# Kernel tuning notes

Hardware: AMD Instinct MI355X
Metric: run time of the kernel (lower is better)

The kernel has to match this reference:

```python
import jax, jax.numpy as jnp
import numpy as np

B, S, D_MODEL, H = 4, 1024, 1024, 16
HD = D_MODEL // H  # head_dim = 64


def setup_inputs() -> dict:
    key = jax.random.key(0)
    ks = jax.random.split(key, 12)
    sd = 1.0 / np.sqrt(D_MODEL)
    return {
        "x": jax.random.normal(ks[0], (B, S, D_MODEL), dtype=jnp.float32),
        "Wq": jax.random.normal(ks[1], (D_MODEL, D_MODEL), dtype=jnp.float32) * sd,
        "bq": jnp.zeros((D_MODEL,), dtype=jnp.float32),
        "Wk": jax.random.normal(ks[2], (D_MODEL, D_MODEL), dtype=jnp.float32) * sd,
        "bk": jnp.zeros((D_MODEL,), dtype=jnp.float32),
        "Wv": jax.random.normal(ks[3], (D_MODEL, D_MODEL), dtype=jnp.float32) * sd,
        "bv": jnp.zeros((D_MODEL,), dtype=jnp.float32),
        "W1": jax.random.normal(ks[4], (2 * D_MODEL, D_MODEL), dtype=jnp.float32) * sd,
        "b1": jnp.zeros((2 * D_MODEL,), dtype=jnp.float32),
        "W2": jax.random.normal(ks[5], (D_MODEL, 2 * D_MODEL), dtype=jnp.float32) * (1.0 / np.sqrt(2 * D_MODEL)),
        "b2": jnp.zeros((D_MODEL,), dtype=jnp.float32),
        "mask": jnp.ones((B, S, S), dtype=jnp.int32),
    }


def reference(x, Wq, bq, Wk, bk, Wv, bv, W1, b1, W2, b2, mask):
    # QKV projections (torch Linear: y = x @ W.T + b), split into heads -> [B,H,S,HD]
    def proj(W, b):
        return (x @ W.T + b).reshape(B, S, H, HD).transpose(0, 2, 1, 3)

    q = proj(Wq, bq)
    k = proj(Wk, bk)
    v = proj(Wv, bv)

    scores = jnp.einsum("bhqd,bhkd->bhqk", q, k) / jnp.sqrt(jnp.float32(HD))
    # mask [B,S,S] broadcast over heads (original does unsqueeze(1).repeat)
    scores = jnp.where(mask[:, None, :, :] == 0, jnp.float32(-1e8), scores)
    probs = jax.nn.softmax(scores, axis=-1)
    ctx = jnp.einsum("bhqk,bhkd->bhqd", probs, v)
    ctx = ctx.transpose(0, 2, 1, 3).reshape(B, S, D_MODEL)

    # out-projection MLP: Linear(d, 2d) -> ReLU -> Linear(2d, d)
    h = jax.nn.relu(ctx @ W1.T + b1)
    return h @ W2.T + b2
```

## Files before the change

kernel.cpp:

```cpp
#include <hip/hip_runtime.h>
#include <hip/hip_bf16.h>
#include <stdint.h>


#define B_ 4
#define S_ 1024
#define DM_ 1024
#define H_ 16
#define HD_ 64

typedef __attribute__((ext_vector_type(8))) short short8;
typedef __attribute__((ext_vector_type(4))) float f32x4;
typedef __attribute__((ext_vector_type(4))) unsigned short ushort4v;

#define GLB_AS(p) ((const __attribute__((address_space(1))) void*)(p))
#define LDS_AS(p) ((__attribute__((address_space(3))) void*)(p))

__device__ __forceinline__ void async_load16(const void* g, void* l) {
  __builtin_amdgcn_global_load_lds(GLB_AS(g), LDS_AS(l), 16, 0, 0);
}

__device__ __forceinline__ unsigned short f2bf(float x) {
  union { float f; unsigned int u; } v; v.f = x;
  unsigned int r = v.u + 0x7fffu + ((v.u >> 16) & 1u);
  return (unsigned short)(r >> 16);
}

#define QSCALE 0.18033688011112042f

struct ConvArgs {
  const float* src[6];
  unsigned short* dst[6];
  int n4[6];
};

__global__ void convert_bf16_kernel(ConvArgs a) {
  const int seg = blockIdx.y;
  const int n4 = a.n4[seg];
  const f32x4* __restrict__ src = (const f32x4*)a.src[seg];
  ushort4v* __restrict__ dst = (ushort4v*)a.dst[seg];
  for (int i = blockIdx.x * blockDim.x + threadIdx.x; i < n4;
       i += gridDim.x * blockDim.x) {
    f32x4 v = src[i];
    ushort4v o;
    o[0] = f2bf(v[0]); o[1] = f2bf(v[1]); o[2] = f2bf(v[2]); o[3] = f2bf(v[3]);
    dst[i] = o;
  }
}

__global__ void pack_mask_kernel(const int* __restrict__ mask,
                                 unsigned long long* __restrict__ bits,
                                 unsigned int* __restrict__ rowflag) {
  const int row = blockIdx.x * 4 + (threadIdx.x >> 6);
  const int lane = threadIdx.x & 63;
  const int* mr = mask + (size_t)row * S_;
  unsigned long long allf = ~0ull;
#pragma unroll
  for (int g = 0; g < 16; ++g) {
    int mv = mr[g * 64 + lane];
    unsigned long long bal = __ballot(mv != 0);
    if (lane == g) bits[(size_t)row * 16 + g] = bal;
    allf &= bal;
  }
  if (lane == 0) rowflag[row] = (allf == ~0ull) ? 1u : 0u;
}

__global__ void concat_bias_kernel(const float* __restrict__ bq,
                                   const float* __restrict__ bk,
                                   const float* __restrict__ bv,
                                   float* __restrict__ cb) {
  int i = blockIdx.x * 256 + threadIdx.x;
  const float* src = (i < 1024) ? bq : (i < 2048) ? bk : bv;
  cb[i] = src[i & 1023];
}

enum { EPI_QKV = 0, EPI_RELU_BF16 = 2, EPI_F32 = 3, EPI_PARTIAL = 4 };

template <int EPI>
__global__ __launch_bounds__(256, 3) void gemm_bt(
    const unsigned short* __restrict__ A, const unsigned short* __restrict__ Bt,
    const float* __restrict__ bias, void* __restrict__ Cp, int M, int N, int K,
    int Kld) {
  __shared__ unsigned short sA[128 * 64];
  __shared__ unsigned short sB[128 * 64];

  const int tid = threadIdx.x;
  const int lane = tid & 63;
  const int wave = tid >> 6;
  const int quad = lane >> 4;
  const int l15 = lane & 15;
  const int swzb = l15 & 7;
  const int m0 = blockIdx.y * 128;
  const int n0 = blockIdx.x * 128;
  const int wm = (wave >> 1) * 64;
  const int wn = (wave & 1) * 64;
  const int kz = blockIdx.z * K;

  f32x4 acc[4][4];
#pragma unroll
  for (int i = 0; i < 4; ++i)
#pragma unroll
    for (int j = 0; j < 4; ++j) acc[i][j] = (f32x4){0.f, 0.f, 0.f, 0.f};

  const int srow = tid >> 3;
  const int scol = ((tid & 7) ^ (srow & 7)) * 8;
  const unsigned short* gA = A + (size_t)(m0 + srow) * Kld + kz + scol;
  const unsigned short* gB = Bt + (size_t)(n0 + srow) * Kld + kz + scol;
  unsigned short* lA = sA + tid * 8;
  unsigned short* lB = sB + tid * 8;

  for (int k0 = 0; k0 < K; k0 += 64) {
    __syncthreads();
#pragma unroll
    for (int st = 0; st < 4; ++st) {
      async_load16(gA + (size_t)(st * 32) * Kld + k0, lA + st * 2048);
      async_load16(gB + (size_t)(st * 32) * Kld + k0, lB + st * 2048);
    }
    __syncthreads();

#pragma unroll
    for (int ks = 0; ks < 2; ++ks) {
      short8 af[4], bfr[4];
#pragma unroll
      for (int t = 0; t < 4; ++t) {
        const int cg = ((ks * 4 + quad) ^ swzb) * 8;
        af[t] = *(const short8*)(sA + (wm + t * 16 + l15) * 64 + cg);
        bfr[t] = *(const short8*)(sB + (wn + t * 16 + l15) * 64 + cg);
      }
#pragma unroll
      for (int mt = 0; mt < 4; ++mt)
#pragma unroll
        for (int nt = 0; nt < 4; ++nt)
          acc[mt][nt] = __builtin_amdgcn_mfma_f32_16x16x32_bf16(
              af[mt], bfr[nt], acc[mt][nt], 0, 0, 0);
    }
  }

#pragma unroll
  for (int nt = 0; nt < 4; ++nt) {
    const int col = n0 + wn + nt * 16 + l15;
    const float bv = (EPI == EPI_PARTIAL) ? 0.f : bias[col];
    const float scl = (EPI == EPI_QKV && col < 1024) ? QSCALE : 1.0f;
#pragma unroll
    for (int mt = 0; mt < 4; ++mt) {
#pragma unroll
      for (int r = 0; r < 4; ++r) {
        const int row = m0 + wm + mt * 16 + quad * 4 + r;
        float v = acc[mt][nt][r] + bv;
        if (EPI == EPI_F32) {
          ((float*)Cp)[(size_t)row * N + col] = v;
        } else if (EPI == EPI_PARTIAL) {
          ((float*)Cp)[(size_t)blockIdx.z * M * N + (size_t)row * N + col] = v;
        } else if (EPI == EPI_RELU_BF16) {
          ((unsigned short*)Cp)[(size_t)row * N + col] = f2bf(fmaxf(v, 0.f));
        } else {
          ((unsigned short*)Cp)[(size_t)row * N + col] = f2bf(v * scl);
        }
      }
    }
  }
}

__global__ __launch_bounds__(256) void transpose_v(
    const unsigned short* __restrict__ Cqkv, unsigned short* __restrict__ Vt) {
  __shared__ unsigned short t[128 * 65];
  const int bh = blockIdx.x;
  const int stile = blockIdx.y;
  const int b = bh >> 4, h = bh & 15;
  const int tid = threadIdx.x;
  const unsigned short* src =
      Cqkv + ((size_t)(b * S_) + stile * 128) * 3072 + 2048 + h * 64;
#pragma unroll
  for (int ps = 0; ps < 4; ++ps) {
    const int idx = ps * 256 + tid;
    const int r = idx >> 3, c = idx & 7;
    const short8 v = *(const short8*)(src + (size_t)r * 3072 + c * 8);
#pragma unroll
    for (int i = 0; i < 8; ++i) t[r * 65 + c * 8 + i] = (unsigned short)v[i];
  }
  __syncthreads();
  unsigned short* dst = Vt + (size_t)bh * HD_ * S_ + stile * 128;
#pragma unroll
  for (int ps = 0; ps < 4; ++ps) {
    const int idx = ps * 256 + tid;
    const int d = idx >> 4, sc = idx & 15;
    short8 v;
#pragma unroll
    for (int i = 0; i < 8; ++i) v[i] = (short)t[(sc * 8 + i) * 65 + d];
    *(short8*)(dst + (size_t)d * S_ + sc * 8) = v;
  }
}

__global__ __launch_bounds__(256, 2) void flash_attn(
    const unsigned short* __restrict__ Cqkv, const unsigned short* __restrict__ Vt,
    const unsigned long long* __restrict__ mbits,
    const unsigned int* __restrict__ mrowflag,
    unsigned short* __restrict__ ctx) {
  __shared__ unsigned short sK[128 * 64];
  __shared__ unsigned short sV[64 * 128];
  __shared__ unsigned short spb[4][32 * 136];

  const int tid = threadIdx.x;
  const int wave = tid >> 6;
  const int lane = tid & 63;
  const int quad = lane >> 4;
  const int l15 = lane & 15;
  const int bh = blockIdx.x;
  const int b = bh >> 4;
  const int h = bh & 15;
  const int qbase = blockIdx.y * 128 + wave * 32;

  const unsigned short* Qb = Cqkv + (size_t)(b * S_) * 3072 + h * HD_;
  const unsigned short* Kb = Cqkv + (size_t)(b * S_) * 3072 + DM_ + h * HD_;
  const unsigned short* Vb = Vt + (size_t)bh * HD_ * S_;
  unsigned short* pbuf = spb[wave];

  bool mask_all_ones;
  {
    unsigned int f = mrowflag[b * S_ + qbase + (lane & 31)];
    mask_all_ones = (__ballot(f != 0) == ~0ull);
  }

  short8 qf[2][2];
#pragma unroll
  for (int u = 0; u < 2; ++u)
#pragma unroll
    for (int ks = 0; ks < 2; ++ks)
      qf[u][ks] = *(const short8*)(Qb + (size_t)(qbase + u * 16 + l15) * 3072 +
                                   ks * 32 + quad * 8);

  f32x4 o[2][4];
#pragma unroll
  for (int u = 0; u < 2; ++u)
#pragma unroll
    for (int i = 0; i < 4; ++i) o[u][i] = (f32x4){0.f, 0.f, 0.f, 0.f};
  float lsum[2][4] = {{0.f, 0.f, 0.f, 0.f}, {0.f, 0.f, 0.f, 0.f}};

  for (int kt = 0; kt < S_ / 128; ++kt) {
    const int kbase = kt * 128;

    __syncthreads();
#pragma unroll
    for (int st = 0; st < 4; ++st) {
      const int j = st * 256 + tid;
      const int r = j >> 3, c = j & 7;
      async_load16(Kb + (size_t)(kbase + r) * 3072 + ((c ^ (r & 7)) * 8),
                   sK + j * 8);
    }
#pragma unroll
    for (int st = 0; st < 4; ++st) {
      const int j = st * 256 + tid;
      const int d = j >> 4, c = j & 15;
      async_load16(Vb + (size_t)d * S_ + kbase + ((c ^ (d & 15)) * 8),
                   sV + j * 8);
    }
    __syncthreads();

    f32x4 s[2][8];
#pragma unroll
    for (int u = 0; u < 2; ++u)
#pragma unroll
      for (int i = 0; i < 8; ++i) s[u][i] = (f32x4){0.f, 0.f, 0.f, 0.f};
#pragma unroll
    for (int ks = 0; ks < 2; ++ks) {
      const int cg = ks * 4 + quad;
#pragma unroll
      for (int nt = 0; nt < 8; ++nt) {
        const int row = nt * 16 + l15;
        const short8 kf =
            *(const short8*)(sK + row * 64 + ((cg ^ (row & 7)) * 8));
        s[0][nt] = __builtin_amdgcn_mfma_f32_16x16x32_bf16(qf[0][ks], kf,
                                                           s[0][nt], 0, 0, 0);
        s[1][nt] = __builtin_amdgcn_mfma_f32_16x16x32_bf16(qf[1][ks], kf,
                                                           s[1][nt], 0, 0, 0);
      }
    }

    if (!mask_all_ones) {
#pragma unroll
      for (int u = 0; u < 2; ++u)
#pragma unroll
        for (int r = 0; r < 4; ++r) {
          const int q = qbase + u * 16 + quad * 4 + r;
          const unsigned long long* wp =
              mbits + ((size_t)(b * S_ + q)) * 16 + kt * 2;
          const unsigned long long w0 = wp[0], w1 = wp[1];
#pragma unroll
          for (int nt = 0; nt < 8; ++nt) {
            const unsigned long long w = (nt < 4) ? w0 : w1;
            const int bit = (nt * 16 + l15) & 63;
            if (!((w >> bit) & 1)) s[u][nt][r] = -1.0e8f;
          }
        }
    }

#pragma unroll
    for (int u = 0; u < 2; ++u)
#pragma unroll
      for (int nt = 0; nt < 8; ++nt)
#pragma unroll
        for (int r = 0; r < 4; ++r) {
          const float p = __builtin_amdgcn_exp2f(s[u][nt][r]);
          lsum[u][r] += p;
          pbuf[(u * 16 + quad * 4 + r) * 136 + nt * 16 + l15] = f2bf(p);
        }

#pragma unroll
    for (int ks2 = 0; ks2 < 4; ++ks2) {
      const short8 pf0 =
          *(const short8*)(pbuf + l15 * 136 + ks2 * 32 + quad * 8);
      const short8 pf1 =
          *(const short8*)(pbuf + (16 + l15) * 136 + ks2 * 32 + quad * 8);
      const int cg = ks2 * 4 + quad;
#pragma unroll
      for (int nt = 0; nt < 4; ++nt) {
        const int d = nt * 16 + l15;
        const short8 vf =
            *(const short8*)(sV + d * 128 + ((cg ^ (d & 15)) * 8));
        o[0][nt] = __builtin_amdgcn_mfma_f32_16x16x32_bf16(pf0, vf, o[0][nt], 0, 0, 0);
        o[1][nt] = __builtin_amdgcn_mfma_f32_16x16x32_bf16(pf1, vf, o[1][nt], 0, 0, 0);
      }
    }
  }

#pragma unroll
  for (int u = 0; u < 2; ++u)
#pragma unroll
    for (int r = 0; r < 4; ++r) {
      float lr = lsum[u][r];
      lr += __shfl_xor(lr, 1);
      lr += __shfl_xor(lr, 2);
      lr += __shfl_xor(lr, 4);
      lr += __shfl_xor(lr, 8);
      const float inv = 1.0f / lr;
#pragma unroll
      for (int nt = 0; nt < 4; ++nt)
        pbuf[(u * 16 + quad * 4 + r) * 68 + nt * 16 + l15] =
            f2bf(o[u][nt][r] * inv);
    }
#pragma unroll
  for (int i = 0; i < 4; ++i) {
    const int j = i * 64 + lane;
    const int r = j >> 3, c = j & 7;
    const short8 val = *(const short8*)(pbuf + r * 68 + c * 8);
    *(short8*)(ctx + ((size_t)b * S_ + qbase + r) * DM_ + h * HD_ + c * 8) = val;
  }
}

__global__ void reduce_ffn2_kernel(const float* __restrict__ part,
                                   const float* __restrict__ b2,
                                   float* __restrict__ out) {
  const int i = blockIdx.x * 256 + threadIdx.x;
  const f32x4 a = ((const f32x4*)part)[i];
  const f32x4 b = ((const f32x4*)part)[i + (B_ * S_ * DM_ / 4)];
  const f32x4 bb = ((const f32x4*)b2)[i & 255];
  ((f32x4*)out)[i] = a + b + bb;
}

extern "C" void kernel_launch(void* const* d_in, const int* in_sizes, int n_in,
                              void* d_out, int out_size, void* d_ws,
                              size_t ws_size, hipStream_t stream) {
  const float* x = (const float*)d_in[0];
  const float* Wq = (const float*)d_in[1];
  const float* bq = (const float*)d_in[2];
  const float* Wk = (const float*)d_in[3];
  const float* bk = (const float*)d_in[4];
  const float* Wv = (const float*)d_in[5];
  const float* bv = (const float*)d_in[6];
  const float* W1 = (const float*)d_in[7];
  const float* b1 = (const float*)d_in[8];
  const float* W2 = (const float*)d_in[9];
  const float* b2 = (const float*)d_in[10];
  const int* mask = (const int*)d_in[11];
  float* out = (float*)d_out;

  char* ws = (char*)d_ws;
  unsigned short* xb   = (unsigned short*)(ws + 0);
  unsigned short* Vt   = (unsigned short*)(ws + 0);
  unsigned short* wqkv = (unsigned short*)(ws + 8388608);
  unsigned short* w1b  = (unsigned short*)(ws + 14680064);
  unsigned short* w2b  = (unsigned short*)(ws + 18874368);
  unsigned short* Cqkv = (unsigned short*)(ws + 23068672);
  unsigned short* ctxb = (unsigned short*)(ws + 48234496);
  unsigned short* hb   = (unsigned short*)(ws + 56623104);
  unsigned long long* mbits = (unsigned long long*)(ws + 73400320);
  unsigned int* mrowflag    = (unsigned int*)(ws + 73924608);
  float* cb                 = (float*)(ws + 73940992);
  float* part = (float*)(ws + 23068672);

  ConvArgs ca;
  ca.src[0] = x;  ca.dst[0] = xb;               ca.n4[0] = (B_ * S_ * DM_) / 4;
  ca.src[1] = Wq; ca.dst[1] = wqkv;             ca.n4[1] = (DM_ * DM_) / 4;
  ca.src[2] = Wk; ca.dst[2] = wqkv + DM_ * DM_; ca.n4[2] = (DM_ * DM_) / 4;
  ca.src[3] = Wv; ca.dst[3] = wqkv + 2 * DM_ * DM_; ca.n4[3] = (DM_ * DM_) / 4;
  ca.src[4] = W1; ca.dst[4] = w1b;              ca.n4[4] = (2 * DM_ * DM_) / 4;
  ca.src[5] = W2; ca.dst[5] = w2b;              ca.n4[5] = (2 * DM_ * DM_) / 4;
  convert_bf16_kernel<<<dim3(256, 6), 256, 0, stream>>>(ca);

  pack_mask_kernel<<<dim3((B_ * S_) / 4), 256, 0, stream>>>(mask, mbits, mrowflag);
  concat_bias_kernel<<<dim3(12), 256, 0, stream>>>(bq, bk, bv, cb);

  const int M = B_ * S_;
  gemm_bt<EPI_QKV><<<dim3(3 * DM_ / 128, M / 128), 256, 0, stream>>>(
      xb, wqkv, cb, Cqkv, M, 3 * DM_, DM_, DM_);

  transpose_v<<<dim3(B_ * H_, S_ / 128), 256, 0, stream>>>(Cqkv, Vt);

  flash_attn<<<dim3(B_ * H_, S_ / 128), 256, 0, stream>>>(
      Cqkv, Vt, mbits, mrowflag, ctxb);

  gemm_bt<EPI_RELU_BF16><<<dim3((2 * DM_) / 128, M / 128), 256, 0, stream>>>(
      ctxb, w1b, b1, hb, M, 2 * DM_, DM_, DM_);

  gemm_bt<EPI_PARTIAL><<<dim3(DM_ / 128, M / 128, 2), 256, 0, stream>>>(
      hb, w2b, b2, part, M, DM_, DM_, 2 * DM_);
  reduce_ffn2_kernel<<<dim3(M * DM_ / 4 / 256), 256, 0, stream>>>(part, b2, out);
}
```

Measured before the change: 246.1 us.

## Fuse V transpose into QKV GEMM epilogue and merge prep kernels

The QKV GEMM blocks that produce V columns now stage their tile in shared memory transposed and write V directly in the [B,H,D,S] layout, which removes the separate transpose_v kernel and its extra read and write of V. The bf16 conversion, mask packing and bias concatenation are merged into one prep kernel launch with extra grid segments. Vt moves to the hb workspace region, and the shared memory array grows to hold the 128x136 transposed tile, which may affect occupancy.

```diff
diff --git a/kernel.cpp b/kernel.cpp
--- a/kernel.cpp
+++ b/kernel.cpp
@@ -28,50 +28,56 @@
 
 #define QSCALE 0.18033688011112042f
 
-struct ConvArgs {
+struct PrepArgs {
   const float* src[6];
   unsigned short* dst[6];
   int n4[6];
+  const int* mask;
+  unsigned long long* bits;
+  unsigned int* rowflag;
+  const float* bq;
+  const float* bk;
+  const float* bv;
+  float* cb;
 };
 
-__global__ void convert_bf16_kernel(ConvArgs a) {
+__global__ void prep_kernel(PrepArgs a) {
   const int seg = blockIdx.y;
-  const int n4 = a.n4[seg];
-  const f32x4* __restrict__ src = (const f32x4*)a.src[seg];
-  ushort4v* __restrict__ dst = (ushort4v*)a.dst[seg];
-  for (int i = blockIdx.x * blockDim.x + threadIdx.x; i < n4;
-       i += gridDim.x * blockDim.x) {
-    f32x4 v = src[i];
-    ushort4v o;
-    o[0] = f2bf(v[0]); o[1] = f2bf(v[1]); o[2] = f2bf(v[2]); o[3] = f2bf(v[3]);
-    dst[i] = o;
-  }
-}
-
-__global__ void pack_mask_kernel(const int* __restrict__ mask,
-                                 unsigned long long* __restrict__ bits,
-                                 unsigned int* __restrict__ rowflag) {
-  const int row = blockIdx.x * 4 + (threadIdx.x >> 6);
-  const int lane = threadIdx.x & 63;
-  const int* mr = mask + (size_t)row * S_;
-  unsigned long long allf = ~0ull;
-#pragma unroll
-  for (int g = 0; g < 16; ++g) {
-    int mv = mr[g * 64 + lane];
-    unsigned long long bal = __ballot(mv != 0);
-    if (lane == g) bits[(size_t)row * 16 + g] = bal;
-    allf &= bal;
-  }
-  if (lane == 0) rowflag[row] = (allf == ~0ull) ? 1u : 0u;
-}
-
-__global__ void concat_bias_kernel(const float* __restrict__ bq,
-                                   const float* __restrict__ bk,
-                                   const float* __restrict__ bv,
-                                   float* __restrict__ cb) {
-  int i = blockIdx.x * 256 + threadIdx.x;
-  const float* src = (i < 1024) ? bq : (i < 2048) ? bk : bv;
-  cb[i] = src[i & 1023];
+  if (seg < 6) {
+    const int n4 = a.n4[seg];
+    const f32x4* __restrict__ src = (const f32x4*)a.src[seg];
+    ushort4v* __restrict__ dst = (ushort4v*)a.dst[seg];
+    for (int i = blockIdx.x * blockDim.x + threadIdx.x; i < n4;
+         i += gridDim.x * blockDim.x) {
+      f32x4 v = src[i];
+      ushort4v o;
+      o[0] = f2bf(v[0]); o[1] = f2bf(v[1]); o[2] = f2bf(v[2]); o[3] = f2bf(v[3]);
+      dst[i] = o;
+    }
+  } else if (seg == 6) {
+    const int wave = threadIdx.x >> 6;
+    const int lane = threadIdx.x & 63;
+#pragma unroll
+    for (int rr = 0; rr < 4; ++rr) {
+      const int row = blockIdx.x * 16 + wave * 4 + rr;
+      const int* mr = a.mask + (size_t)row * S_;
+      unsigned long long allf = ~0ull;
+#pragma unroll
+      for (int g = 0; g < 16; ++g) {
+        int mv = mr[g * 64 + lane];
+        unsigned long long bal = __ballot(mv != 0);
+        if (lane == g) a.bits[(size_t)row * 16 + g] = bal;
+        allf &= bal;
+      }
+      if (lane == 0) a.rowflag[row] = (allf == ~0ull) ? 1u : 0u;
+    }
+  } else {
+    const int i = blockIdx.x * 256 + threadIdx.x;
+    if (i < 3072) {
+      const float* src = (i < 1024) ? a.bq : (i < 2048) ? a.bk : a.bv;
+      a.cb[i] = src[i & 1023];
+    }
+  }
 }
 
 enum { EPI_QKV = 0, EPI_RELU_BF16 = 2, EPI_F32 = 3, EPI_PARTIAL = 4 };
@@ -79,10 +85,11 @@
 template <int EPI>
 __global__ __launch_bounds__(256, 3) void gemm_bt(
     const unsigned short* __restrict__ A, const unsigned short* __restrict__ Bt,
-    const float* __restrict__ bias, void* __restrict__ Cp, int M, int N, int K,
-    int Kld) {
-  __shared__ unsigned short sA[128 * 64];
-  __shared__ unsigned short sB[128 * 64];
+    const float* __restrict__ bias, void* __restrict__ Cp,
+    unsigned short* __restrict__ Vt, int M, int N, int K, int Kld) {
+  __shared__ __align__(16) unsigned short smem[128 * 136];
+  unsigned short* sA = smem;
+  unsigned short* sB = smem + 128 * 64;
 
   const int tid = threadIdx.x;
   const int lane = tid & 63;
@@ -134,6 +141,36 @@
           acc[mt][nt] = __builtin_amdgcn_mfma_f32_16x16x32_bf16(
               af[mt], bfr[nt], acc[mt][nt], 0, 0, 0);
     }
+  }
+
+  if (EPI == EPI_QKV && n0 >= 2048) {
+    __syncthreads();
+#pragma unroll
+    for (int nt = 0; nt < 4; ++nt) {
+      const int col = n0 + wn + nt * 16 + l15;
+      const float bv = bias[col];
+#pragma unroll
+      for (int mt = 0; mt < 4; ++mt)
+#pragma unroll
+        for (int r = 0; r < 4; ++r)
+          smem[(wn + nt * 16 + l15) * 136 + wm + mt * 16 + quad * 4 + r] =
+              f2bf(acc[mt][nt][r] + bv);
+    }
+    __syncthreads();
+    const int vc0 = n0 - 2048;
+    const int bb = m0 >> 10;
+    const int s0 = m0 & 1023;
+#pragma unroll
+    for (int i = 0; i < 8; ++i) {
+      const int c = i * 16 + (tid >> 4);
+      const int tc = tid & 15;
+      const short8 val = *(const short8*)(smem + c * 136 + tc * 8);
+      const int ch = vc0 + c;
+      const int hh = ch >> 6, dd = ch & 63;
+      *(short8*)(Vt + ((size_t)(bb * 16 + hh) * HD_ + dd) * S_ + s0 + tc * 8) =
+          val;
+    }
+    return;
   }
 
 #pragma unroll
@@ -158,36 +195,6 @@
         }
       }
     }
-  }
-}
-
-__global__ __launch_bounds__(256) void transpose_v(
-    const unsigned short* __restrict__ Cqkv, unsigned short* __restrict__ Vt) {
-  __shared__ unsigned short t[128 * 65];
-  const int bh = blockIdx.x;
-  const int stile = blockIdx.y;
-  const int b = bh >> 4, h = bh & 15;
-  const int tid = threadIdx.x;
-  const unsigned short* src =
-      Cqkv + ((size_t)(b * S_) + stile * 128) * 3072 + 2048 + h * 64;
-#pragma unroll
-  for (int ps = 0; ps < 4; ++ps) {
-    const int idx = ps * 256 + tid;
-    const int r = idx >> 3, c = idx & 7;
-    const short8 v = *(const short8*)(src + (size_t)r * 3072 + c * 8);
-#pragma unroll
-    for (int i = 0; i < 8; ++i) t[r * 65 + c * 8 + i] = (unsigned short)v[i];
-  }
-  __syncthreads();
-  unsigned short* dst = Vt + (size_t)bh * HD_ * S_ + stile * 128;
-#pragma unroll
-  for (int ps = 0; ps < 4; ++ps) {
-    const int idx = ps * 256 + tid;
-    const int d = idx >> 4, sc = idx & 15;
-    short8 v;
-#pragma unroll
-    for (int i = 0; i < 8; ++i) v[i] = (short)t[(sc * 8 + i) * 65 + d];
-    *(short8*)(dst + (size_t)d * S_ + sc * 8) = v;
   }
 }
 
@@ -376,43 +383,40 @@
 
   char* ws = (char*)d_ws;
   unsigned short* xb   = (unsigned short*)(ws + 0);
-  unsigned short* Vt   = (unsigned short*)(ws + 0);
   unsigned short* wqkv = (unsigned short*)(ws + 8388608);
   unsigned short* w1b  = (unsigned short*)(ws + 14680064);
   unsigned short* w2b  = (unsigned short*)(ws + 18874368);
   unsigned short* Cqkv = (unsigned short*)(ws + 23068672);
   unsigned short* ctxb = (unsigned short*)(ws + 48234496);
   unsigned short* hb   = (unsigned short*)(ws + 56623104);
+  unsigned short* Vt   = (unsigned short*)(ws + 56623104);
   unsigned long long* mbits = (unsigned long long*)(ws + 73400320);
   unsigned int* mrowflag    = (unsigned int*)(ws + 73924608);
   float* cb                 = (float*)(ws + 73940992);
   float* part = (float*)(ws + 23068672);
 
-  ConvArgs ca;
-  ca.src[0] = x;  ca.dst[0] = xb;               ca.n4[0] = (B_ * S_ * DM_) / 4;
-  ca.src[1] = Wq; ca.dst[1] = wqkv;             ca.n4[1] = (DM_ * DM_) / 4;
-  ca.src[2] = Wk; ca.dst[2] = wqkv + DM_ * DM_; ca.n4[2] = (DM_ * DM_) / 4;
-  ca.src[3] = Wv; ca.dst[3] = wqkv + 2 * DM_ * DM_; ca.n4[3] = (DM_ * DM_) / 4;
-  ca.src[4] = W1; ca.dst[4] = w1b;              ca.n4[4] = (2 * DM_ * DM_) / 4;
-  ca.src[5] = W2; ca.dst[5] = w2b;              ca.n4[5] = (2 * DM_ * DM_) / 4;
-  convert_bf16_kernel<<<dim3(256, 6), 256, 0, stream>>>(ca);
-
-  pack_mask_kernel<<<dim3((B_ * S_) / 4), 256, 0, stream>>>(mask, mbits, mrowflag);
-  concat_bias_kernel<<<dim3(12), 256, 0, stream>>>(bq, bk, bv, cb);
+  PrepArgs pa;
+  pa.src[0] = x;  pa.dst[0] = xb;               pa.n4[0] = (B_ * S_ * DM_) / 4;
+  pa.src[1] = Wq; pa.dst[1] = wqkv;             pa.n4[1] = (DM_ * DM_) / 4;
+  pa.src[2] = Wk; pa.dst[2] = wqkv + DM_ * DM_; pa.n4[2] = (DM_ * DM_) / 4;
+  pa.src[3] = Wv; pa.dst[3] = wqkv + 2 * DM_ * DM_; pa.n4[3] = (DM_ * DM_) / 4;
+  pa.src[4] = W1; pa.dst[4] = w1b;              pa.n4[4] = (2 * DM_ * DM_) / 4;
+  pa.src[5] = W2; pa.dst[5] = w2b;              pa.n4[5] = (2 * DM_ * DM_) / 4;
+  pa.mask = mask; pa.bits = mbits; pa.rowflag = mrowflag;
+  pa.bq = bq; pa.bk = bk; pa.bv = bv; pa.cb = cb;
+  prep_kernel<<<dim3(256, 8), 256, 0, stream>>>(pa);
 
   const int M = B_ * S_;
   gemm_bt<EPI_QKV><<<dim3(3 * DM_ / 128, M / 128), 256, 0, stream>>>(
-      xb, wqkv, cb, Cqkv, M, 3 * DM_, DM_, DM_);
-
-  transpose_v<<<dim3(B_ * H_, S_ / 128), 256, 0, stream>>>(Cqkv, Vt);
+      xb, wqkv, cb, Cqkv, Vt, M, 3 * DM_, DM_, DM_);
 
   flash_attn<<<dim3(B_ * H_, S_ / 128), 256, 0, stream>>>(
       Cqkv, Vt, mbits, mrowflag, ctxb);
 
   gemm_bt<EPI_RELU_BF16><<<dim3((2 * DM_) / 128, M / 128), 256, 0, stream>>>(
-      ctxb, w1b, b1, hb, M, 2 * DM_, DM_, DM_);
+      ctxb, w1b, b1, hb, nullptr, M, 2 * DM_, DM_, DM_);
 
   gemm_bt<EPI_PARTIAL><<<dim3(DM_ / 128, M / 128, 2), 256, 0, stream>>>(
-      hb, w2b, b2, part, M, DM_, DM_, 2 * DM_);
+      hb, w2b, b2, part, nullptr, M, DM_, DM_, 2 * DM_);
   reduce_ffn2_kernel<<<dim3(M * DM_ / 4 / 256), 256, 0, stream>>>(part, b2, out);
 }
```

New measurement: 256.0 us. +4.0%, slower.
